# Performance work log

Hardware: AMD Instinct MI355X
Metric: run time of the kernel (lower is better)

## Reference

```python
import jax, jax.numpy as jnp
import numpy as np

EPS = 1e-8


def setup_inputs() -> dict:
    key = jax.random.key(0)
    k1, k2, k3 = jax.random.split(key, 3)
    B, N, K, D = 64, 4096, 64, 256
    x = jax.random.normal(k1, (B, N, D), dtype=jnp.float32)
    mu = jax.random.normal(k2, (K, D), dtype=jnp.float32)
    log_sigma = jax.random.normal(k3, (K, D), dtype=jnp.float32) * 0.1
    return {"x": x, "mu": mu, "log_sigma": log_sigma, "n_slots": 8}


def reference(x, mu, log_sigma, n_slots):
    # cosine similarity: normalize then contract (avoids [B,N,K,D] broadcast)
    xn = x / jnp.maximum(jnp.linalg.norm(x, axis=-1, keepdims=True), EPS)
    mn = mu / jnp.maximum(jnp.linalg.norm(mu, axis=-1, keepdims=True), EPS)
    cos = jnp.einsum('bnd,kd->bnk', xn, mn)            # [B, N, K]
    cos_soft = jax.nn.softmax(cos, axis=-1)            # softmax over concepts
    r = jax.nn.softmax(cos_soft.sum(axis=1), axis=-1)  # [B, K]
    _, idx = jax.lax.top_k(r, n_slots)                 # [B, n_slots]
    mu_sample = mu[idx]                                # [B, n_slots, D]
    sigma_sample = jnp.exp(log_sigma[idx])             # [B, n_slots, D]
    noise = jax.random.normal(jax.random.key(42), mu_sample.shape, dtype=mu_sample.dtype)
    return mu_sample + sigma_sample * noise
```

## Files before the change

kernel.cpp:

```cpp
#include <hip/hip_runtime.h>
#include <math.h>
#include <stdint.h>

#define B_ 64
#define N_ 4096
#define K_ 64
#define D_ 256
#define NS_ 8

__device__ __forceinline__ float fadd(float a, float b) { return __fadd_rn(a, b); }
__device__ __forceinline__ float fmul(float a, float b) { return __fmul_rn(a, b); }

__device__ __forceinline__ float np_expf(float x) {
  const float LOG2E = 1.442695040888963407359924681001892137f;
  float qf = rintf(__fmul_rn(x, LOG2E));
  float r = __fmaf_rn(qf, -6.93145752e-1f, x);
  r = __fmaf_rn(qf, -1.42860677e-6f, r);
  float num = __fmaf_rn(r, 5.082762527590693718096e-04f, 6.757896990527504603057e-03f);
  num = __fmaf_rn(num, r, 5.114512081637298353406e-02f);
  num = __fmaf_rn(num, r, 2.473615434895520810817e-01f);
  num = __fmaf_rn(num, r, 7.257664613233124478488e-01f);
  num = __fmaf_rn(num, r, 9.999999999980870924916e-01f);
  float den = __fmaf_rn(r, 2.159509375685829852307e-02f, -2.742335390411667452936e-01f);
  den = __fmaf_rn(den, r, 1.000000000000000000000e+00f);
  float poly = __fdiv_rn(num, den);
  int qi = (int)qf;
  float scale = __int_as_float((127 + qi) << 23);
  return __fmul_rn(poly, scale);
}

__device__ __forceinline__ uint32_t rotl32(uint32_t x, int r) {
  return (x << r) | (x >> (32 - r));
}
__device__ __forceinline__ float jax_normal_from_index(uint32_t i) {
  uint32_t x0 = 0u, x1 = i;
  const uint32_t ks0 = 0u, ks1 = 42u, ks2 = 0x1BD11BDAu ^ 0u ^ 42u;
  x0 += ks0; x1 += ks1;
#define TF_ROUND(r) { x0 += x1; x1 = rotl32(x1, (r)); x1 ^= x0; }
  TF_ROUND(13) TF_ROUND(15) TF_ROUND(26) TF_ROUND(6)
  x0 += ks1; x1 += ks2 + 1u;
  TF_ROUND(17) TF_ROUND(29) TF_ROUND(16) TF_ROUND(24)
  x0 += ks2; x1 += ks0 + 2u;
  TF_ROUND(13) TF_ROUND(15) TF_ROUND(26) TF_ROUND(6)
  x0 += ks0; x1 += ks1 + 3u;
  TF_ROUND(17) TF_ROUND(29) TF_ROUND(16) TF_ROUND(24)
  x0 += ks1; x1 += ks2 + 4u;
  TF_ROUND(13) TF_ROUND(15) TF_ROUND(26) TF_ROUND(6)
  x0 += ks2; x1 += ks0 + 5u;
#undef TF_ROUND
  uint32_t bits = x0 ^ x1;
  uint32_t fb = (bits >> 9) | 0x3f800000u;
  float f = __uint_as_float(fb) - 1.0f;
  const float lo = __uint_as_float(0xBF7FFFFFu);
  float u = f * 2.0f + lo;
  u = fmaxf(lo, u);
  float w = -log1pf(-u * u);
  float p;
  if (w < 5.0f) {
    w = w - 2.5f;
    p = 2.81022636e-08f;
    p = fmaf(p, w, 3.43273939e-07f);
    p = fmaf(p, w, -3.5233877e-06f);
    p = fmaf(p, w, -4.39150654e-06f);
    p = fmaf(p, w, 0.00021858087f);
    p = fmaf(p, w, -0.00125372503f);
    p = fmaf(p, w, -0.00417768164f);
    p = fmaf(p, w, 0.246640727f);
    p = fmaf(p, w, 1.50140941f);
  } else {
    w = sqrtf(w) - 3.0f;
    p = -0.000200214257f;
    p = fmaf(p, w, 0.000100950558f);
    p = fmaf(p, w, 0.00134934322f);
    p = fmaf(p, w, -0.00367342844f);
    p = fmaf(p, w, 0.00573950773f);
    p = fmaf(p, w, -0.0076224613f);
    p = fmaf(p, w, 0.00943887047f);
    p = fmaf(p, w, 1.00167406f);
    p = fmaf(p, w, 2.83297682f);
  }
  return 1.41421356f * (p * u);
}

__device__ __forceinline__ float np_pw128_sq(const float* p) {
  float t16[16];
#pragma unroll
  for (int L = 0; L < 16; ++L) {
    float q0 = p[L];       q0 = fmul(q0, q0);
    float q1 = p[L + 16];  q1 = fmul(q1, q1);
    float q2 = p[L + 32];  q2 = fmul(q2, q2);
    float q3 = p[L + 48];  q3 = fmul(q3, q3);
    float q4 = p[L + 64];  q4 = fmul(q4, q4);
    float q5 = p[L + 80];  q5 = fmul(q5, q5);
    float q6 = p[L + 96];  q6 = fmul(q6, q6);
    float q7 = p[L + 112]; q7 = fmul(q7, q7);
    t16[L] = fadd(fadd(fadd(q0, q4), fadd(q1, q5)), fadd(fadd(q2, q6), fadd(q3, q7)));
  }
  float u8[8];
#pragma unroll
  for (int L = 0; L < 8; ++L) u8[L] = fadd(t16[L], t16[L + 8]);
  float v4[4];
#pragma unroll
  for (int L = 0; L < 4; ++L) v4[L] = fadd(u8[L], u8[L + 4]);
  return fadd(fadd(v4[0], v4[2]), fadd(v4[1], v4[3]));
}

__device__ __forceinline__ float np_sum64(const float* a) {
  float t16[16];
#pragma unroll
  for (int L = 0; L < 16; ++L)
    t16[L] = fadd(fadd(a[L], a[16 + L]), fadd(a[32 + L], a[48 + L]));
  float u8[8];
#pragma unroll
  for (int L = 0; L < 8; ++L) u8[L] = fadd(t16[L], t16[L + 8]);
  float v4[4];
#pragma unroll
  for (int L = 0; L < 4; ++L) v4[L] = fadd(u8[L], u8[L + 4]);
  return fadd(fadd(v4[0], v4[2]), fadd(v4[1], v4[3]));
}

__global__ __launch_bounds__(64)
void prep_mnT(const float* __restrict__ mu, float4* __restrict__ mnT4) {
  const int k = threadIdx.x;
  const float* mrow = mu + k * D_;
  const float n2 = fadd(np_pw128_sq(mrow), np_pw128_sq(mrow + 128));
  const float den = fmaxf(__fsqrt_rn(n2), 1e-8f);
#pragma unroll 8
  for (int t = 0; t < 64; ++t) {
    float4 m = *(const float4*)&mrow[4 * t];
    float4 o;
    o.x = __fdiv_rn(m.x, den); o.y = __fdiv_rn(m.y, den);
    o.z = __fdiv_rn(m.z, den); o.w = __fdiv_rn(m.w, den);
    mnT4[t * K_ + k] = o;
  }
}

__global__ __launch_bounds__(512, 1)
void xn_cos_softmax(const float* __restrict__ x,
                    const float4* __restrict__ mnT4_g,
                    float* __restrict__ p_ws) {
  __shared__ float4 mnT4[64][64];
  __shared__ float xst[8][8][256];
  __shared__ float dnorm[8][8];

  const int b = blockIdx.x;
  const int seg = blockIdx.y;
  const int tid = threadIdx.x;
  const int w = tid >> 6;
  const int lane = tid & 63;

#pragma unroll
  for (int i = 0; i < 8; ++i)
    ((float4*)mnT4)[tid * 8 + i] = mnT4_g[tid * 8 + i];
  __syncthreads();

  const int L16 = lane & 15;
  const int rowg = lane >> 4;

  for (int pass = 0; pass < 8; ++pass) {
    const int n0 = seg * 512 + w * 64 + pass * 8;

#pragma unroll
    for (int r = 0; r < 8; ++r) {
      const float4 v = *(const float4*)&x[(((size_t)b << 12) + n0 + r) * D_ + lane * 4];
      *(float4*)&xst[w][r][lane * 4] = v;
    }
    __syncthreads();

#pragma unroll
    for (int hs = 0; hs < 2; ++hs) {
      const int r = hs * 4 + rowg;
      const float* rowp = &xst[w][r][0];
      float res2[2];
#pragma unroll
      for (int half = 0; half < 2; ++half) {
        const float* p = rowp + half * 128 + L16;
        float q0 = p[0];   q0 = fmul(q0, q0);
        float q1 = p[16];  q1 = fmul(q1, q1);
        float q2 = p[32];  q2 = fmul(q2, q2);
        float q3 = p[48];  q3 = fmul(q3, q3);
        float q4 = p[64];  q4 = fmul(q4, q4);
        float q5 = p[80];  q5 = fmul(q5, q5);
        float q6 = p[96];  q6 = fmul(q6, q6);
        float q7 = p[112]; q7 = fmul(q7, q7);
        const float t = fadd(fadd(fadd(q0, q4), fadd(q1, q5)),
                             fadd(fadd(q2, q6), fadd(q3, q7)));
        float u  = fadd(t, __shfl_xor(t, 8));
        float v  = fadd(u, __shfl_xor(u, 4));
        float w2 = fadd(v, __shfl_xor(v, 2));
        res2[half] = fadd(w2, __shfl_xor(w2, 1));
      }
      if (L16 == 0) {
        const float n2 = fadd(res2[0], res2[1]);
        dnorm[w][r] = fmaxf(__fsqrt_rn(n2), 1e-8f);
      }
    }
    __syncthreads();

#pragma unroll
    for (int r = 0; r < 8; ++r) {
      const float den = dnorm[w][r];
      float4 v = *(float4*)&xst[w][r][lane * 4];
      v.x = __fdiv_rn(v.x, den); v.y = __fdiv_rn(v.y, den);
      v.z = __fdiv_rn(v.z, den); v.w = __fdiv_rn(v.w, den);
      *(float4*)&xst[w][r][lane * 4] = v;
    }
    __syncthreads();

    float acc[8][4];
#pragma unroll
    for (int r = 0; r < 8; ++r)
#pragma unroll
      for (int j = 0; j < 4; ++j) acc[r][j] = 0.f;

#pragma unroll 4
    for (int t = 0; t < 64; ++t) {
      const float4 m4 = mnT4[t][lane];
#pragma unroll
      for (int r = 0; r < 8; ++r) {
        const float4 x4 = *(const float4*)&xst[w][r][4 * t];
        acc[r][0] = fadd(acc[r][0], fmul(x4.x, m4.x));
        acc[r][1] = fadd(acc[r][1], fmul(x4.y, m4.y));
        acc[r][2] = fadd(acc[r][2], fmul(x4.z, m4.z));
        acc[r][3] = fadd(acc[r][3], fmul(x4.w, m4.w));
      }
    }

#pragma unroll
    for (int r = 0; r < 8; ++r) {
      const float cosr = fadd(fadd(acc[r][0], acc[r][1]), fadd(acc[r][2], acc[r][3]));
      float mx = cosr;
      mx = fmaxf(mx, __shfl_xor(mx, 1));
      mx = fmaxf(mx, __shfl_xor(mx, 2));
      mx = fmaxf(mx, __shfl_xor(mx, 4));
      mx = fmaxf(mx, __shfl_xor(mx, 8));
      mx = fmaxf(mx, __shfl_xor(mx, 16));
      mx = fmaxf(mx, __shfl_xor(mx, 32));
      const float e = np_expf(__fsub_rn(cosr, mx));
      float g1 = fadd(e, __shfl_xor(e, 16));
      float g2 = fadd(g1, __shfl_xor(g1, 32));
      float u  = fadd(g2, __shfl_xor(g2, 8));
      float v  = fadd(u, __shfl_xor(u, 4));
      float w2 = fadd(v, __shfl_xor(v, 2));
      float sres = fadd(w2, __shfl_xor(w2, 1));
      const float denom = __shfl(sres, 0);
      const float p = __fdiv_rn(e, denom);
      p_ws[(((size_t)b << 12) + n0 + r) * K_ + lane] = p;
    }
    __syncthreads();
  }
}

__global__ __launch_bounds__(256)
void pairwise_sum_n(const float* __restrict__ p_ws, float* __restrict__ s) {
  __shared__ float part[4][K_];
  const int b = blockIdx.x;
  const int w = threadIdx.x >> 6;
  const int k = threadIdx.x & 63;
  const float* base = p_ws + ((size_t)b << 12) * K_ + k;

  float l[8];
#pragma unroll 1
  for (int i = 0; i < 8; ++i) {
    const float* leaf = base + (size_t)(w * 8 + i) * 128 * K_;
    float c[16];
#pragma unroll
    for (int L = 0; L < 16; ++L) {
      const float* pL = leaf + (size_t)L * K_;
      const float q0 = pL[0 * 16 * K_];
      const float q1 = pL[1 * 16 * K_];
      const float q2 = pL[2 * 16 * K_];
      const float q3 = pL[3 * 16 * K_];
      const float q4 = pL[4 * 16 * K_];
      const float q5 = pL[5 * 16 * K_];
      const float q6 = pL[6 * 16 * K_];
      const float q7 = pL[7 * 16 * K_];
      c[L] = fadd(fadd(fadd(q0, q4), fadd(q1, q5)), fadd(fadd(q2, q6), fadd(q3, q7)));
    }
    float u8[8];
#pragma unroll
    for (int L = 0; L < 8; ++L) u8[L] = fadd(c[L], c[L + 8]);
    float v4[4];
#pragma unroll
    for (int L = 0; L < 4; ++L) v4[L] = fadd(u8[L], u8[L + 4]);
    l[i] = fadd(fadd(v4[0], v4[2]), fadd(v4[1], v4[3]));
  }
  const float Sw = fadd(fadd(fadd(l[0], l[1]), fadd(l[2], l[3])),
                        fadd(fadd(l[4], l[5]), fadd(l[6], l[7])));
  part[w][k] = Sw;
  __syncthreads();
  if (w == 0) {
    const float root = fadd(fadd(part[0][k], part[1][k]), fadd(part[2][k], part[3][k]));
    s[b * K_ + k] = root;
  }
}

__global__ __launch_bounds__(256)
void topk_sample(const float* __restrict__ s,
                 const float* __restrict__ mu,
                 const float* __restrict__ ls,
                 float* __restrict__ out) {
  __shared__ float sv[K_];
  __shared__ int sidx[NS_];
  const int b = blockIdx.x;
  const int t = threadIdx.x;
  if (t < K_) sv[t] = s[b * K_ + t];
  __syncthreads();
  if (t == 0) {
    float mx = sv[0];
    for (int k = 1; k < K_; ++k) mx = fmaxf(mx, sv[k]);
    float e[K_];
    for (int k = 0; k < K_; ++k) e[k] = np_expf(__fsub_rn(sv[k], mx));
    const float denom = np_sum64(e);
    float rv[K_];
    for (int k = 0; k < K_; ++k) rv[k] = __fdiv_rn(e[k], denom);
    for (int q = 0; q < NS_; ++q) {
      float best = -1.0e30f; int bi = 0;
      for (int k = 0; k < K_; ++k) {
        if (rv[k] > best) { best = rv[k]; bi = k; }
      }
      sidx[q] = bi;
      rv[bi] = -1.0e30f;
    }
  }
  __syncthreads();

  const int q = t >> 5;
  const int d0 = (t & 31) * 8;
  const int k = sidx[q];
  const float* mrow = mu + k * D_ + d0;
  const float* lrow = ls + k * D_ + d0;
  float* orow = out + ((size_t)b * NS_ + q) * D_ + d0;
  const uint32_t ibase = (uint32_t)(((b * NS_) + q) * D_ + d0);
#pragma unroll
  for (int j = 0; j < 8; ++j) {
    const float z = jax_normal_from_index(ibase + (uint32_t)j);
    orow[j] = fmaf(expf(lrow[j]), z, mrow[j]);
  }
}

extern "C" void kernel_launch(void* const* d_in, const int* in_sizes, int n_in,
                              void* d_out, int out_size, void* d_ws, size_t ws_size,
                              hipStream_t stream) {
  const float* x  = (const float*)d_in[0];
  const float* mu = (const float*)d_in[1];
  const float* ls = (const float*)d_in[2];
  float* out = (float*)d_out;
  (void)ws_size; (void)in_sizes; (void)n_in; (void)out_size;

  float*  p_ws = (float*)d_ws;
  float*  s    = (float*)((char*)d_ws + (size_t)67108864);
  float4* mnT4 = (float4*)((char*)d_ws + (size_t)67125248);

  prep_mnT<<<1, 64, 0, stream>>>(mu, mnT4);
  dim3 grid(B_, 8);
  xn_cos_softmax<<<grid, 512, 0, stream>>>(x, mnT4, p_ws);
  pairwise_sum_n<<<B_, 256, 0, stream>>>(p_ws, s);
  topk_sample<<<B_, 256, 0, stream>>>(s, mu, ls, out);
}
```

Measured before the change: 333.2 us.

## Widen cos-softmax blocks to 1024 threads and split the N reduction across blocks

The cosine/softmax kernel moves to 1024-thread blocks, each wave handling 4 rows per pass instead of 8. Row norms are now passed between lanes with shuffles rather than through a shared dnorm array. The N-sum kernel is split into 4 groups per batch, writing partial sums that topk_sample adds up, which gives 256 blocks instead of 64. This raises parallelism and latency hiding, but each wave reuses the mu fragment over fewer rows and the final summation order changes slightly.

```diff
diff --git a/kernel.cpp b/kernel.cpp
--- a/kernel.cpp
+++ b/kernel.cpp
@@ -135,13 +135,12 @@
   }
 }
 
-__global__ __launch_bounds__(512, 1)
+__global__ __launch_bounds__(1024, 1)
 void xn_cos_softmax(const float* __restrict__ x,
                     const float4* __restrict__ mnT4_g,
                     float* __restrict__ p_ws) {
   __shared__ float4 mnT4[64][64];
-  __shared__ float xst[8][8][256];
-  __shared__ float dnorm[8][8];
+  __shared__ float xst[16][4][256];
 
   const int b = blockIdx.x;
   const int seg = blockIdx.y;
@@ -150,27 +149,26 @@
   const int lane = tid & 63;
 
 #pragma unroll
-  for (int i = 0; i < 8; ++i)
-    ((float4*)mnT4)[tid * 8 + i] = mnT4_g[tid * 8 + i];
+  for (int i = 0; i < 4; ++i)
+    ((float4*)mnT4)[tid * 4 + i] = mnT4_g[tid * 4 + i];
   __syncthreads();
 
   const int L16 = lane & 15;
   const int rowg = lane >> 4;
 
   for (int pass = 0; pass < 8; ++pass) {
-    const int n0 = seg * 512 + w * 64 + pass * 8;
-
-#pragma unroll
-    for (int r = 0; r < 8; ++r) {
+    const int n0 = seg * 512 + pass * 64 + w * 4;
+
+#pragma unroll
+    for (int r = 0; r < 4; ++r) {
       const float4 v = *(const float4*)&x[(((size_t)b << 12) + n0 + r) * D_ + lane * 4];
       *(float4*)&xst[w][r][lane * 4] = v;
     }
     __syncthreads();
 
-#pragma unroll
-    for (int hs = 0; hs < 2; ++hs) {
-      const int r = hs * 4 + rowg;
-      const float* rowp = &xst[w][r][0];
+    float den4[4];
+    {
+      const float* rowp = &xst[w][rowg][0];
       float res2[2];
 #pragma unroll
       for (int half = 0; half < 2; ++half) {
@@ -190,26 +188,25 @@
         float w2 = fadd(v, __shfl_xor(v, 2));
         res2[half] = fadd(w2, __shfl_xor(w2, 1));
       }
-      if (L16 == 0) {
-        const float n2 = fadd(res2[0], res2[1]);
-        dnorm[w][r] = fmaxf(__fsqrt_rn(n2), 1e-8f);
-      }
+      const float n2 = fadd(res2[0], res2[1]);
+      const float den = fmaxf(__fsqrt_rn(n2), 1e-8f);
+#pragma unroll
+      for (int r = 0; r < 4; ++r) den4[r] = __shfl(den, 16 * r);
     }
     __syncthreads();
 
 #pragma unroll
-    for (int r = 0; r < 8; ++r) {
-      const float den = dnorm[w][r];
+    for (int r = 0; r < 4; ++r) {
       float4 v = *(float4*)&xst[w][r][lane * 4];
-      v.x = __fdiv_rn(v.x, den); v.y = __fdiv_rn(v.y, den);
-      v.z = __fdiv_rn(v.z, den); v.w = __fdiv_rn(v.w, den);
+      v.x = __fdiv_rn(v.x, den4[r]); v.y = __fdiv_rn(v.y, den4[r]);
+      v.z = __fdiv_rn(v.z, den4[r]); v.w = __fdiv_rn(v.w, den4[r]);
       *(float4*)&xst[w][r][lane * 4] = v;
     }
     __syncthreads();
 
-    float acc[8][4];
-#pragma unroll
-    for (int r = 0; r < 8; ++r)
+    float acc[4][4];
+#pragma unroll
+    for (int r = 0; r < 4; ++r)
 #pragma unroll
       for (int j = 0; j < 4; ++j) acc[r][j] = 0.f;
 
@@ -217,7 +214,7 @@
     for (int t = 0; t < 64; ++t) {
       const float4 m4 = mnT4[t][lane];
 #pragma unroll
-      for (int r = 0; r < 8; ++r) {
+      for (int r = 0; r < 4; ++r) {
         const float4 x4 = *(const float4*)&xst[w][r][4 * t];
         acc[r][0] = fadd(acc[r][0], fmul(x4.x, m4.x));
         acc[r][1] = fadd(acc[r][1], fmul(x4.y, m4.y));
@@ -227,7 +224,7 @@
     }
 
 #pragma unroll
-    for (int r = 0; r < 8; ++r) {
+    for (int r = 0; r < 4; ++r) {
       const float cosr = fadd(fadd(acc[r][0], acc[r][1]), fadd(acc[r][2], acc[r][3]));
       float mx = cosr;
       mx = fmaxf(mx, __shfl_xor(mx, 1));
@@ -252,17 +249,18 @@
 }
 
 __global__ __launch_bounds__(256)
-void pairwise_sum_n(const float* __restrict__ p_ws, float* __restrict__ s) {
+void pairwise_sum_n(const float* __restrict__ p_ws, float* __restrict__ s_part) {
   __shared__ float part[4][K_];
   const int b = blockIdx.x;
+  const int g = blockIdx.y;
   const int w = threadIdx.x >> 6;
   const int k = threadIdx.x & 63;
   const float* base = p_ws + ((size_t)b << 12) * K_ + k;
 
-  float l[8];
+  float l[2];
 #pragma unroll 1
-  for (int i = 0; i < 8; ++i) {
-    const float* leaf = base + (size_t)(w * 8 + i) * 128 * K_;
+  for (int i = 0; i < 2; ++i) {
+    const float* leaf = base + (size_t)(g * 8 + w * 2 + i) * 128 * K_;
     float c[16];
 #pragma unroll
     for (int L = 0; L < 16; ++L) {
@@ -285,18 +283,16 @@
     for (int L = 0; L < 4; ++L) v4[L] = fadd(u8[L], u8[L + 4]);
     l[i] = fadd(fadd(v4[0], v4[2]), fadd(v4[1], v4[3]));
   }
-  const float Sw = fadd(fadd(fadd(l[0], l[1]), fadd(l[2], l[3])),
-                        fadd(fadd(l[4], l[5]), fadd(l[6], l[7])));
-  part[w][k] = Sw;
+  part[w][k] = fadd(l[0], l[1]);
   __syncthreads();
   if (w == 0) {
-    const float root = fadd(fadd(part[0][k], part[1][k]), fadd(part[2][k], part[3][k]));
-    s[b * K_ + k] = root;
+    const float Sg = fadd(fadd(part[0][k], part[1][k]), fadd(part[2][k], part[3][k]));
+    s_part[(b * 4 + g) * K_ + k] = Sg;
   }
 }
 
 __global__ __launch_bounds__(256)
-void topk_sample(const float* __restrict__ s,
+void topk_sample(const float* __restrict__ s_part,
                  const float* __restrict__ mu,
                  const float* __restrict__ ls,
                  float* __restrict__ out) {
@@ -304,7 +300,13 @@
   __shared__ int sidx[NS_];
   const int b = blockIdx.x;
   const int t = threadIdx.x;
-  if (t < K_) sv[t] = s[b * K_ + t];
+  if (t < K_) {
+    const float S0 = s_part[(b * 4 + 0) * K_ + t];
+    const float S1 = s_part[(b * 4 + 1) * K_ + t];
+    const float S2 = s_part[(b * 4 + 2) * K_ + t];
+    const float S3 = s_part[(b * 4 + 3) * K_ + t];
+    sv[t] = fadd(fadd(S0, S1), fadd(S2, S3));
+  }
   __syncthreads();
   if (t == 0) {
     float mx = sv[0];
@@ -348,13 +350,14 @@
   float* out = (float*)d_out;
   (void)ws_size; (void)in_sizes; (void)n_in; (void)out_size;
 
-  float*  p_ws = (float*)d_ws;
-  float*  s    = (float*)((char*)d_ws + (size_t)67108864);
-  float4* mnT4 = (float4*)((char*)d_ws + (size_t)67125248);
+  float*  p_ws   = (float*)d_ws;
+  float*  s_part = (float*)((char*)d_ws + (size_t)67108864);
+  float4* mnT4   = (float4*)((char*)d_ws + (size_t)67174400);
 
   prep_mnT<<<1, 64, 0, stream>>>(mu, mnT4);
   dim3 grid(B_, 8);
-  xn_cos_softmax<<<grid, 512, 0, stream>>>(x, mnT4, p_ws);
-  pairwise_sum_n<<<B_, 256, 0, stream>>>(p_ws, s);
-  topk_sample<<<B_, 256, 0, stream>>>(s, mu, ls, out);
-}
+  xn_cos_softmax<<<grid, 1024, 0, stream>>>(x, mnT4, p_ws);
+  dim3 grid2(B_, 4);
+  pairwise_sum_n<<<grid2, 256, 0, stream>>>(p_ws, s_part);
+  topk_sample<<<B_, 256, 0, stream>>>(s_part, mu, ls, out);
+}
```

Result: faster. 325.1 us (-2.4%).
